# Optimization experiments

Hardware: AMD Instinct MI355X
Metric: run time of the kernel (lower is better)

## Reference

```python
import jax, jax.numpy as jnp
import numpy as np

K_FACTOR = 8
TOP_N = 4
NUM_LAYER = 2


def setup_inputs() -> dict:
    key = jax.random.key(0)
    ks = jax.random.split(key, 5)
    num_ent, num_rel, n_edges = 50000, 500, 500000
    emb_dim = 128
    emb_s = emb_dim // K_FACTOR  # 16
    ent_embeddings = jax.random.normal(ks[0], (num_ent, emb_dim), jnp.float32)
    rel_embeddings = jax.random.normal(ks[1], (num_rel, TOP_N * emb_s), jnp.float32)
    rel_att = jax.random.normal(ks[2], (num_rel, K_FACTOR), jnp.float32)
    edge_index = jax.random.randint(ks[3], (2, n_edges), 0, num_ent)
    edge_type = jax.random.randint(ks[4], (n_edges,), 0, num_rel)
    return dict(ent_embeddings=ent_embeddings, rel_embeddings=rel_embeddings,
                rel_att=rel_att, edge_index=edge_index, edge_type=edge_type,
                num_ent=num_ent, num_rel=num_rel)


def _segment_mean(src, idx, n):
    s = jax.ops.segment_sum(src, idx, num_segments=n)
    c = jax.ops.segment_sum(jnp.ones((src.shape[0],), src.dtype), idx, num_segments=n)
    return jnp.where(c[:, None] > 0, s / jnp.maximum(c, 1.0)[:, None], 0.0)


def _conv(x, r, r_att, ei, et, num_ent, num_rel):
    emb_dim = x.shape[1]
    s = emb_dim // K_FACTOR
    # add self-loop edges with relation id num_rel (zero embedding / zero att)
    loop = jnp.arange(num_ent, dtype=ei.dtype)
    ei = jnp.concatenate([ei, jnp.stack([loop, loop])], axis=1)
    et = jnp.concatenate([et, jnp.full((num_ent,), num_rel, et.dtype)])
    r_pad = jnp.concatenate([r, jnp.zeros((1, r.shape[1]), r.dtype)], axis=0)
    ra_pad = jnp.concatenate([r_att, jnp.zeros((1, K_FACTOR), r_att.dtype)], axis=0)

    neigh_t = x[ei[1]]          # (E, D)
    neigh_h = x[ei[0]]          # (E, D)
    neigh_r = r_pad[et]         # (E, top_n*s)
    att = jax.nn.softmax(ra_pad[et], axis=1)      # (E, k)
    order = jnp.argsort(-att, axis=-1)             # descending sort indices
    top, rem = order[:, :TOP_N], order[:, TOP_N:]

    E = neigh_h.shape[0]
    tf = neigh_t.reshape(E, K_FACTOR, s)
    hf = neigh_h.reshape(E, K_FACTOR, s)
    t_top = jnp.take_along_axis(tf, top[:, :, None], axis=1)  # (E, top_n, s)
    h_top = jnp.take_along_axis(hf, top[:, :, None], axis=1)
    h_rem = jnp.take_along_axis(hf, rem[:, :, None], axis=1)

    tmp = (h_top.reshape(E, -1) + neigh_r).reshape(E, TOP_N, s)
    rows = jnp.arange(E)[:, None]
    # the fresh random ent_embed in the original is fully overwritten by the
    # two scatters (top + remaining cover all k_factor slots) -> deterministic
    ent = (jnp.zeros((E, K_FACTOR, s), x.dtype)
           .at[rows, top].set(tmp)
           .at[rows, rem].set(h_rem))

    ent_embed = _segment_mean(ent.reshape(E, emb_dim), ei[1], num_ent)
    rel_embed = _segment_mean(t_top.reshape(E, -1) - h_top.reshape(E, -1), et, num_rel + 1)
    return jax.nn.relu(ent_embed), rel_embed[:-1], r_att


def reference(ent_embeddings, rel_embeddings, rel_att, edge_index, edge_type, num_ent, num_rel):
    x, r = ent_embeddings, rel_embeddings
    for _ in range(NUM_LAYER):
        # faithful to MAE.forward: the ORIGINAL rel_att is passed to every layer
        x, r, _ = _conv(x, r, rel_att, edge_index, edge_type, num_ent, num_rel)
    return (x, r)
```

## Files before the change

kernel.cpp:

```cpp
#include <hip/hip_runtime.h>

#define KF 8
#define TN 4
#define SDIM 16
#define EMB 128
#define NS 8
#define NB 128
#define NT 512
#define NRMAX 512
#define SCE 1024

typedef unsigned int u32;

__device__ __forceinline__ u32 pack2bf(float a, float b) {
    u32 ua = __float_as_uint(a), ub = __float_as_uint(b);
    ua = (ua + 0x7FFFu + ((ua >> 16) & 1u)) >> 16;
    ub = (ub + 0x7FFFu + ((ub >> 16) & 1u)) >> 16;
    return ua | (ub << 16);
}
__device__ __forceinline__ float lo16(u32 w) { return __uint_as_float(w << 16); }
__device__ __forceinline__ float hi16(u32 w) { return __uint_as_float(w & 0xFFFF0000u); }

__global__ __launch_bounds__(256) void k_init(int* __restrict__ deg, int num_ent,
                                              int* __restrict__ rcnt, int num_rel,
                                              float* __restrict__ rsumA, float* __restrict__ rsumB,
                                              int nrsum) {
    int i = blockIdx.x * 256 + threadIdx.x;
    if (i < num_ent) deg[i] = 0;
    if (i < num_rel) rcnt[i] = 0;
    if (i < nrsum) { rsumA[i] = 0.f; rsumB[i] = 0.f; }
}

__global__ __launch_bounds__(256) void k_hist(const int* __restrict__ tails, const int* __restrict__ types,
                                              int nE, int num_rel,
                                              int* __restrict__ deg, int* __restrict__ rcnt) {
    __shared__ int hist[NRMAX];
    for (int q = threadIdx.x; q < num_rel; q += 256) hist[q] = 0;
    __syncthreads();
    for (int i = blockIdx.x * 256 + threadIdx.x; i < nE; i += gridDim.x * 256) {
        atomicAdd(&deg[tails[i]], 1);
        atomicAdd(&hist[types[i]], 1);
    }
    __syncthreads();
    for (int q = threadIdx.x; q < num_rel; q += 256) {
        int h = hist[q];
        if (h) atomicAdd(&rcnt[q], h);
    }
}

__device__ void scan_small(const int* __restrict__ in, int* __restrict__ out, int* __restrict__ out2, int n) {
    __shared__ int warp_sums[16];
    int carry = 0;
    int lane = threadIdx.x & 63, wid = threadIdx.x >> 6;
    int nw = blockDim.x >> 6;
    for (int base = 0; base < n; base += blockDim.x) {
        int i = base + (int)threadIdx.x;
        int v = (i < n) ? in[i] : 0;
        int sv = v;
        for (int o = 1; o < 64; o <<= 1) { int t = __shfl_up(sv, o, 64); if (lane >= o) sv += t; }
        if (lane == 63) warp_sums[wid] = sv;
        __syncthreads();
        if (wid == 0 && lane < nw) {
            int ws = warp_sums[lane];
            for (int o = 1; o < 16; o <<= 1) { int t = __shfl_up(ws, o, 64); if (lane >= o) ws += t; }
            warp_sums[lane] = ws;
        }
        __syncthreads();
        int wofs = (wid > 0) ? warp_sums[wid - 1] : 0;
        int total = warp_sums[nw - 1];
        if (i < n) {
            int e = carry + wofs + sv - v;
            out[i] = e;
            if (out2) out2[i] = e;
        }
        carry += total;
        __syncthreads();
    }
    if (threadIdx.x == 0) out[n] = carry;
}

__global__ void k_scan_pair(const int* __restrict__ bsum, int* __restrict__ bofs, int nblk,
                            const int* __restrict__ rcnt, int* __restrict__ rel_off,
                            int* __restrict__ rel_cur, int num_rel) {
    if (blockIdx.x == 0) scan_small(bsum, bofs, nullptr, nblk);
    else                 scan_small(rcnt, rel_off, rel_cur, num_rel);
}

__global__ __launch_bounds__(256) void k_scan1(const int* __restrict__ in, int* __restrict__ out,
                                               int* __restrict__ bsum, int n) {
    __shared__ int warp_sums[4];
    int blk = blockIdx.x;
    int i0 = blk * SCE + (int)threadIdx.x * 4;
    int v[4];
#pragma unroll
    for (int j = 0; j < 4; ++j) { int i = i0 + j; v[j] = (i < n) ? in[i] : 0; }
    int tsum = v[0] + v[1] + v[2] + v[3];
    int lane = threadIdx.x & 63, wid = threadIdx.x >> 6;
    int sv = tsum;
    for (int o = 1; o < 64; o <<= 1) { int t = __shfl_up(sv, o, 64); if (lane >= o) sv += t; }
    if (lane == 63) warp_sums[wid] = sv;
    __syncthreads();
    if (threadIdx.x == 0) {
        int s = 0;
        for (int w = 0; w < 4; ++w) { int t = warp_sums[w]; warp_sums[w] = s; s += t; }
        bsum[blk] = s;
    }
    __syncthreads();
    int run = warp_sums[wid] + sv - tsum;
#pragma unroll
    for (int j = 0; j < 4; ++j) { int i = i0 + j; if (i < n) out[i] = run; run += v[j]; }
}

__global__ __launch_bounds__(256) void k_scan2(int* __restrict__ out, int* __restrict__ out2,
                                               const int* __restrict__ bofs, int n, int nblk) {
    int blk = blockIdx.x;
    int add = bofs[blk];
    int i0 = blk * SCE + (int)threadIdx.x * 4;
#pragma unroll
    for (int j = 0; j < 4; ++j) {
        int i = i0 + j;
        if (i < n) { int val = out[i] + add; out[i] = val; out2[i] = val; }
    }
    if (blk == 0 && threadIdx.x == 0) out[n] = bofs[nblk];
}

__global__ __launch_bounds__(256) void k_scatter_fused(
        const int* __restrict__ heads, const int* __restrict__ tails, const int* __restrict__ types,
        int nE, int num_ent, int num_rel,
        int* __restrict__ tail_cur, u32* __restrict__ tail_edges,
        int* __restrict__ rel_cur, u32* __restrict__ rel_edges,
        const float4* __restrict__ x4, u32* __restrict__ xh, int n4,
        const float* __restrict__ rel_att, const float* __restrict__ r0,
        int* __restrict__ posmap, int* __restrict__ topmap, u32* __restrict__ pr0,
        int nc, int np) {
    int bid = blockIdx.x;
    if (bid < NT) {
        int xcd = bid & 7;
        int w = bid >> 3;
        int nw = NT >> 3;
        int per = (num_ent + 7) >> 3;
        int lo = xcd * per, hi = min(lo + per, num_ent);
        for (int i = w * 256 + (int)threadIdx.x; i < nE; i += nw * 256) {
            int t = tails[i];
            if (t >= lo && t < hi) {
                int p = atomicAdd(&tail_cur[t], 1);
                tail_edges[p] = (u32)heads[i] | ((u32)types[i] << 16);
            }
        }
    } else if (bid < NT + NB) {
        __shared__ int hist[NRMAX];
        __shared__ int base[NRMAX];
        int bi = bid - NT;
        int c = (bi & 7) * (NB >> 3) + (bi >> 3);
        int chunk = (nE + NB - 1) / NB;
        int beg = c * chunk, end = min(beg + chunk, nE);
        for (int q = threadIdx.x; q < num_rel; q += 256) hist[q] = 0;
        __syncthreads();
        for (int i = beg + (int)threadIdx.x; i < end; i += 256) atomicAdd(&hist[types[i]], 1);
        __syncthreads();
        for (int q = threadIdx.x; q < num_rel; q += 256) {
            int h = hist[q];
            base[q] = h > 0 ? atomicAdd(&rel_cur[q], h) : 0;
            hist[q] = 0;
        }
        __syncthreads();
        for (int i = beg + (int)threadIdx.x; i < end; i += 256) {
            int q = types[i];
            int rank = atomicAdd(&hist[q], 1);
            rel_edges[base[q] + rank] = (u32)tails[i] | ((u32)heads[i] << 16);
        }
    } else if (bid < NT + NB + nc) {
        int i = (bid - NT - NB) * 256 + (int)threadIdx.x;
        if (i < n4) {
            float4 v = x4[i];
            ((uint2*)xh)[i] = make_uint2(pack2bf(v.x, v.y), pack2bf(v.z, v.w));
        }
    } else {
        int q = (bid - NT - NB - nc) * 4 + ((int)threadIdx.x >> 6);
        if (q >= num_rel) return;
        int i = threadIdx.x & 63;
        float v[KF]; int idx[KF];
        for (int k = 0; k < KF; ++k) { v[k] = rel_att[q * KF + k]; idx[k] = k; }
        for (int a = 1; a < KF; ++a) {
            float va = v[a]; int ia = idx[a]; int j = a - 1;
            while (j >= 0 && v[j] < va) { v[j + 1] = v[j]; idx[j + 1] = idx[j]; --j; }
            v[j + 1] = va; idx[j + 1] = ia;
        }
        int pos[KF];
        for (int k = 0; k < KF; ++k) pos[k] = -1;
        for (int j = 0; j < TN; ++j) pos[idx[j]] = j;
        if (i < KF) posmap[q * KF + i] = pos[i];
        if (i < TN) topmap[q * TN + i] = idx[i];
        int k = i >> 3;
        int p = pos[k];
        u32 w = 0;
        if (p >= 0) {
            float a = r0[q * 64 + p * SDIM + ((2 * i) & 15)];
            float b = r0[q * 64 + p * SDIM + ((2 * i + 1) & 15)];
            w = pack2bf(a, b);
        }
        pr0[q * 64 + i] = w;
    }
}

__global__ __launch_bounds__(256) void k_rel_pass(const u32* __restrict__ xh,
                                                  const int* __restrict__ rel_off,
                                                  const u32* __restrict__ rel_edges,
                                                  const int* __restrict__ topmap,
                                                  float* __restrict__ rsum_top) {
    int bid = blockIdx.x;
    int q = bid >> 3, s = bid & 7;
    int lane = threadIdx.x & 63;
    int qw = lane >> 4, c = lane & 15;
    int wid = threadIdx.x >> 6;
    int k = topmap[q * TN + (c >> 2)];
    int woff = k * 8 + (c & 3) * 2;
    int beg = rel_off[q], end = rel_off[q + 1];
    float acc[4] = {0.f, 0.f, 0.f, 0.f};
    for (int e = beg + s * 16 + wid * 4 + qw; e < end; e += 128) {
        u32 ew = rel_edges[e];
        int t = (int)(ew & 0xFFFFu);
        int h = (int)(ew >> 16);
        uint2 ta = *(const uint2*)(xh + ((size_t)t << 6) + woff);
        uint2 hb = *(const uint2*)(xh + ((size_t)h << 6) + woff);
        acc[0] += lo16(ta.x) - lo16(hb.x);
        acc[1] += hi16(ta.x) - hi16(hb.x);
        acc[2] += lo16(ta.y) - lo16(hb.y);
        acc[3] += hi16(ta.y) - hi16(hb.y);
    }
#pragma unroll
    for (int d = 0; d < 4; ++d) {
        acc[d] += __shfl_xor(acc[d], 16, 64);
        acc[d] += __shfl_xor(acc[d], 32, 64);
    }
    __shared__ float prt[4][64];
    if (qw == 0) {
#pragma unroll
        for (int d = 0; d < 4; ++d) prt[wid][c * 4 + d] = acc[d];
    }
    __syncthreads();
    int tid = threadIdx.x;
    if (tid < 64) {
        float v = prt[0][tid] + prt[1][tid] + prt[2][tid] + prt[3][tid];
        atomicAdd(&rsum_top[(size_t)q * 64 + tid], v);
    }
}

template <bool OUT_BF16>
__global__ __launch_bounds__(256) void k_ent_pass(const u32* __restrict__ xh, const u32* __restrict__ prh,
                                                  const int* __restrict__ tail_off,
                                                  const u32* __restrict__ tail_edges,
                                                  u32* __restrict__ xout_h, float4* __restrict__ xout_f,
                                                  int num_ent) {
    int wid = threadIdx.x >> 6;
    int t = blockIdx.x * 4 + wid;
    if (t >= num_ent) return;
    int lane = threadIdx.x & 63;
    int qw = lane >> 4, c = lane & 15;
    int beg = tail_off[t], end = tail_off[t + 1];
    int deg = end - beg;
    float acc[8] = {0.f, 0.f, 0.f, 0.f, 0.f, 0.f, 0.f, 0.f};
    for (int b2 = 0; b2 < deg; b2 += 64) {
        int m = min(64, deg - b2);
        u32 ew = (lane < m) ? tail_edges[beg + b2 + lane] : 0u;
        for (int j = 0; j < m; j += 4) {
            int idx = j + qw;
            u32 w = __shfl(ew, idx, 64);
            uint4 xr = make_uint4(0, 0, 0, 0), pr = make_uint4(0, 0, 0, 0);
            if (idx < m) {
                int h = (int)(w & 0xFFFFu);
                int q = (int)(w >> 16);
                xr = *(const uint4*)(xh + ((size_t)h << 6) + (c << 2));
                pr = *(const uint4*)(prh + ((size_t)q << 6) + (c << 2));
            }
            acc[0] += lo16(xr.x) + lo16(pr.x);
            acc[1] += hi16(xr.x) + hi16(pr.x);
            acc[2] += lo16(xr.y) + lo16(pr.y);
            acc[3] += hi16(xr.y) + hi16(pr.y);
            acc[4] += lo16(xr.z) + lo16(pr.z);
            acc[5] += hi16(xr.z) + hi16(pr.z);
            acc[6] += lo16(xr.w) + lo16(pr.w);
            acc[7] += hi16(xr.w) + hi16(pr.w);
        }
    }
#pragma unroll
    for (int d = 0; d < 8; ++d) {
        acc[d] += __shfl_xor(acc[d], 16, 64);
        acc[d] += __shfl_xor(acc[d], 32, 64);
    }
    if (qw == 0) {
        uint4 sw = *(const uint4*)(xh + ((size_t)t << 6) + (c << 2));
        float s[8] = { lo16(sw.x), hi16(sw.x), lo16(sw.y), hi16(sw.y),
                       lo16(sw.z), hi16(sw.z), lo16(sw.w), hi16(sw.w) };
        float inv = 1.f / (float)(deg + 1);
        float o[8];
#pragma unroll
        for (int d = 0; d < 8; ++d) {
            float v = (acc[d] + s[d]) * inv;
            o[d] = v > 0.f ? v : 0.f;
        }
        if (OUT_BF16) {
            uint4 ow = make_uint4(pack2bf(o[0], o[1]), pack2bf(o[2], o[3]),
                                  pack2bf(o[4], o[5]), pack2bf(o[6], o[7]));
            *(uint4*)(xout_h + ((size_t)t << 6) + (c << 2)) = ow;
        } else {
            xout_f[((size_t)t << 5) + (c << 1)]     = make_float4(o[0], o[1], o[2], o[3]);
            xout_f[((size_t)t << 5) + (c << 1) + 1] = make_float4(o[4], o[5], o[6], o[7]);
        }
    }
}

__global__ __launch_bounds__(64) void k_relfin_pr(const float* __restrict__ rsum_top,
                                                  const int* __restrict__ rel_off,
                                                  const int* __restrict__ posmap,
                                                  u32* __restrict__ prh, int num_rel) {
    int q = blockIdx.x;
    if (q >= num_rel) return;
    int i = threadIdx.x;
    int k = i >> 3;
    int pos = posmap[q * KF + k];
    int cnt = rel_off[q + 1] - rel_off[q];
    u32 w = 0;
    if (pos >= 0 && cnt > 0) {
        float inv = 1.f / (float)cnt;
        int d0 = (2 * i) & 15;
        float a = rsum_top[(size_t)q * 64 + pos * SDIM + d0] * inv;
        float b = rsum_top[(size_t)q * 64 + pos * SDIM + d0 + 1] * inv;
        w = pack2bf(a, b);
    }
    prh[q * 64 + i] = w;
}

__global__ __launch_bounds__(64) void k_relfin(const float* __restrict__ rsum_top,
                                               const int* __restrict__ rel_off,
                                               float* __restrict__ rout) {
    int q = blockIdx.x;
    int t = threadIdx.x;
    int cnt = rel_off[q + 1] - rel_off[q];
    rout[q * 64 + t] = cnt > 0 ? rsum_top[(size_t)q * 64 + t] / (float)cnt : 0.f;
}

extern "C" void kernel_launch(void* const* d_in, const int* in_sizes, int n_in,
                              void* d_out, int out_size, void* d_ws, size_t ws_size,
                              hipStream_t stream) {
    const float* x0 = (const float*)d_in[0];
    const float* r0 = (const float*)d_in[1];
    const float* rel_att = (const float*)d_in[2];
    const int* edge_index = (const int*)d_in[3];
    const int* edge_type = (const int*)d_in[4];

    const int num_ent = in_sizes[0] / EMB;
    const int num_rel = in_sizes[2] / KF;
    const int nE = in_sizes[4];

    const int* heads = edge_index;
    const int* tails = edge_index + nE;

    const int nblk = (num_ent + SCE - 1) / SCE;
    const int n4 = num_ent * 32;
    const int nc = (n4 + 255) / 256;
    const int np = (num_rel + 3) / 4;

    char* base = (char*)d_ws;
    size_t off = 0;
    auto carve = [&](size_t bytes) { char* p = base + off; off = (off + bytes + 255) & ~(size_t)255; return p; };
    int* deg        = (int*)carve((size_t)num_ent * 4);
    int* tail_off   = (int*)carve((size_t)(num_ent + 1) * 4);
    int* tail_cur   = (int*)carve((size_t)num_ent * 4);
    u32* tail_edges = (u32*)carve((size_t)nE * 4);
    int* rcnt       = (int*)carve((size_t)num_rel * 4);
    int* rel_off    = (int*)carve((size_t)(num_rel + 1) * 4);
    int* rel_cur    = (int*)carve((size_t)num_rel * 4);
    u32* rel_edges  = (u32*)carve((size_t)nE * 4);
    int* posmap     = (int*)carve((size_t)num_rel * KF * 4);
    int* topmap     = (int*)carve((size_t)num_rel * TN * 4);
    int* bsum       = (int*)carve((size_t)nblk * 4);
    int* bofs       = (int*)carve((size_t)(nblk + 1) * 4);
    u32* x0h        = (u32*)carve((size_t)num_ent * EMB * 2);
    u32* x1h        = (u32*)carve((size_t)num_ent * EMB * 2);
    u32* pr0        = (u32*)carve((size_t)num_rel * 64 * 4);
    u32* pr1        = (u32*)carve((size_t)num_rel * 64 * 4);
    float* rsumA    = (float*)carve((size_t)num_rel * 64 * 4);
    float* rsumB    = (float*)carve((size_t)num_rel * 64 * 4);
    (void)ws_size;

    float* x_out = (float*)d_out;
    float* r_out = (float*)d_out + (size_t)num_ent * EMB;

    int initmax = num_ent > num_rel * 64 ? num_ent : num_rel * 64;
    k_init<<<(initmax + 255) / 256, 256, 0, stream>>>(deg, num_ent, rcnt, num_rel,
                                                      rsumA, rsumB, num_rel * 64);
    k_hist<<<256, 256, 0, stream>>>(tails, edge_type, nE, num_rel, deg, rcnt);
    k_scan1<<<nblk, 256, 0, stream>>>(deg, tail_off, bsum, num_ent);
    k_scan_pair<<<2, 1024, 0, stream>>>(bsum, bofs, nblk, rcnt, rel_off, rel_cur, num_rel);
    k_scan2<<<nblk, 256, 0, stream>>>(tail_off, tail_cur, bofs, num_ent, nblk);
    k_scatter_fused<<<NT + NB + nc + np, 256, 0, stream>>>(
        heads, tails, edge_type, nE, num_ent, num_rel,
        tail_cur, tail_edges, rel_cur, rel_edges,
        (const float4*)x0, x0h, n4, rel_att, r0, posmap, topmap, pr0, nc, np);

    int egrid = (num_ent + 3) / 4;

    k_rel_pass<<<num_rel * NS, 256, 0, stream>>>(x0h, rel_off, rel_edges, topmap, rsumA);
    k_ent_pass<true><<<egrid, 256, 0, stream>>>(x0h, pr0, tail_off, tail_edges, x1h, nullptr, num_ent);
    k_relfin_pr<<<num_rel, 64, 0, stream>>>(rsumA, rel_off, posmap, pr1, num_rel);

    k_rel_pass<<<num_rel * NS, 256, 0, stream>>>(x1h, rel_off, rel_edges, topmap, rsumB);
    k_ent_pass<false><<<egrid, 256, 0, stream>>>(x1h, pr1, tail_off, tail_edges, nullptr, (float4*)x_out, num_ent);
    k_relfin<<<num_rel, 64, 0, stream>>>(rsumB, rel_off, r_out);
}
```

Measured before the change: 195.7 us.

## Fuse three-pass scan into decoupled-lookback scan and fold relation finalize into ent pass

Replaces the scan1/scan_pair/scan2 sequence with a single kernel that publishes per-block sums with flags and has each block spin on its predecessors, with one extra block doing the relation-count scan. The relation finalize kernels (relfin_pr, relfin) are folded into the tail of the entity-pass grids as extra blocks. This removes four kernel launches and their inter-kernel gaps. The spin-wait scan relies on earlier blocks being scheduled, and each block serially reads all prior block sums.

```diff
diff --git a/kernel.cpp b/kernel.cpp
--- a/kernel.cpp
+++ b/kernel.cpp
@@ -24,11 +24,12 @@
 __global__ __launch_bounds__(256) void k_init(int* __restrict__ deg, int num_ent,
                                               int* __restrict__ rcnt, int num_rel,
                                               float* __restrict__ rsumA, float* __restrict__ rsumB,
-                                              int nrsum) {
+                                              int nrsum, int* __restrict__ flags, int nblk) {
     int i = blockIdx.x * 256 + threadIdx.x;
     if (i < num_ent) deg[i] = 0;
     if (i < num_rel) rcnt[i] = 0;
     if (i < nrsum) { rsumA[i] = 0.f; rsumB[i] = 0.f; }
+    if (i < nblk) flags[i] = 0;
 }
 
 __global__ __launch_bounds__(256) void k_hist(const int* __restrict__ tails, const int* __restrict__ types,
@@ -79,49 +80,54 @@
     if (threadIdx.x == 0) out[n] = carry;
 }
 
-__global__ void k_scan_pair(const int* __restrict__ bsum, int* __restrict__ bofs, int nblk,
-                            const int* __restrict__ rcnt, int* __restrict__ rel_off,
-                            int* __restrict__ rel_cur, int num_rel) {
-    if (blockIdx.x == 0) scan_small(bsum, bofs, nullptr, nblk);
-    else                 scan_small(rcnt, rel_off, rel_cur, num_rel);
-}
-
-__global__ __launch_bounds__(256) void k_scan1(const int* __restrict__ in, int* __restrict__ out,
-                                               int* __restrict__ bsum, int n) {
-    __shared__ int warp_sums[4];
-    int blk = blockIdx.x;
-    int i0 = blk * SCE + (int)threadIdx.x * 4;
+__global__ __launch_bounds__(256) void k_scan_fused(const int* __restrict__ deg,
+                                                    int* __restrict__ tail_off, int* __restrict__ tail_cur,
+                                                    int n, int nblk,
+                                                    int* __restrict__ vals, int* __restrict__ flags,
+                                                    const int* __restrict__ rcnt, int* __restrict__ rel_off,
+                                                    int* __restrict__ rel_cur, int num_rel) {
+    int b = blockIdx.x;
+    if (b == nblk) { scan_small(rcnt, rel_off, rel_cur, num_rel); return; }
+    __shared__ int wsum[4];
+    __shared__ int pw[4];
+    __shared__ int sprefix;
+    int tid = threadIdx.x;
+    int lane = tid & 63, wid = tid >> 6;
+    int i0 = b * SCE + tid * 4;
     int v[4];
 #pragma unroll
-    for (int j = 0; j < 4; ++j) { int i = i0 + j; v[j] = (i < n) ? in[i] : 0; }
+    for (int j = 0; j < 4; ++j) { int i = i0 + j; v[j] = (i < n) ? deg[i] : 0; }
     int tsum = v[0] + v[1] + v[2] + v[3];
-    int lane = threadIdx.x & 63, wid = threadIdx.x >> 6;
     int sv = tsum;
     for (int o = 1; o < 64; o <<= 1) { int t = __shfl_up(sv, o, 64); if (lane >= o) sv += t; }
-    if (lane == 63) warp_sums[wid] = sv;
-    __syncthreads();
-    if (threadIdx.x == 0) {
+    if (lane == 63) wsum[wid] = sv;
+    __syncthreads();
+    if (tid == 0) {
         int s = 0;
-        for (int w = 0; w < 4; ++w) { int t = warp_sums[w]; warp_sums[w] = s; s += t; }
-        bsum[blk] = s;
-    }
-    __syncthreads();
-    int run = warp_sums[wid] + sv - tsum;
-#pragma unroll
-    for (int j = 0; j < 4; ++j) { int i = i0 + j; if (i < n) out[i] = run; run += v[j]; }
-}
-
-__global__ __launch_bounds__(256) void k_scan2(int* __restrict__ out, int* __restrict__ out2,
-                                               const int* __restrict__ bofs, int n, int nblk) {
-    int blk = blockIdx.x;
-    int add = bofs[blk];
-    int i0 = blk * SCE + (int)threadIdx.x * 4;
+        for (int w = 0; w < 4; ++w) { int t = wsum[w]; wsum[w] = s; s += t; }
+        vals[b] = s;
+        __threadfence();
+        atomicExch(&flags[b], 1);
+    }
+    __syncthreads();
+    int p = 0;
+    for (int i = tid; i < b; i += 256) {
+        while (atomicAdd(&flags[i], 0) == 0) {}
+        p += atomicAdd(&vals[i], 0);
+    }
+    for (int o = 1; o < 64; o <<= 1) p += __shfl_xor(p, o, 64);
+    if (lane == 0) pw[wid] = p;
+    __syncthreads();
+    if (tid == 0) sprefix = pw[0] + pw[1] + pw[2] + pw[3];
+    __syncthreads();
+    int run = sprefix + wsum[wid] + (sv - tsum);
 #pragma unroll
     for (int j = 0; j < 4; ++j) {
         int i = i0 + j;
-        if (i < n) { int val = out[i] + add; out[i] = val; out2[i] = val; }
-    }
-    if (blk == 0 && threadIdx.x == 0) out[n] = bofs[nblk];
+        if (i < n) { tail_off[i] = run; tail_cur[i] = run; }
+        run += v[j];
+    }
+    if (b == nblk - 1 && tid == 0) tail_off[n] = sprefix + vals[b];
 }
 
 __global__ __launch_bounds__(256) void k_scatter_fused(
@@ -251,9 +257,42 @@
                                                   const int* __restrict__ tail_off,
                                                   const u32* __restrict__ tail_edges,
                                                   u32* __restrict__ xout_h, float4* __restrict__ xout_f,
-                                                  int num_ent) {
+                                                  int num_ent, int egrid,
+                                                  const float* __restrict__ rsum_top,
+                                                  const int* __restrict__ rel_off,
+                                                  const int* __restrict__ posmap,
+                                                  u32* __restrict__ pr_out, float* __restrict__ rout,
+                                                  int num_rel) {
+    int bid = blockIdx.x;
+    if (bid >= egrid) {
+        if (OUT_BF16) {
+            int q = (bid - egrid) * 4 + ((int)threadIdx.x >> 6);
+            if (q >= num_rel) return;
+            int i = threadIdx.x & 63;
+            int k = i >> 3;
+            int pos = posmap[q * KF + k];
+            int cnt = rel_off[q + 1] - rel_off[q];
+            u32 w = 0;
+            if (pos >= 0 && cnt > 0) {
+                float inv = 1.f / (float)cnt;
+                int d0 = (2 * i) & 15;
+                float a = rsum_top[(size_t)q * 64 + pos * SDIM + d0] * inv;
+                float b = rsum_top[(size_t)q * 64 + pos * SDIM + d0 + 1] * inv;
+                w = pack2bf(a, b);
+            }
+            pr_out[q * 64 + i] = w;
+        } else {
+            int idx = (bid - egrid) * 256 + (int)threadIdx.x;
+            if (idx < num_rel * 64) {
+                int q = idx >> 6;
+                int cnt = rel_off[q + 1] - rel_off[q];
+                rout[idx] = cnt > 0 ? rsum_top[idx] / (float)cnt : 0.f;
+            }
+        }
+        return;
+    }
     int wid = threadIdx.x >> 6;
-    int t = blockIdx.x * 4 + wid;
+    int t = bid * 4 + wid;
     if (t >= num_ent) return;
     int lane = threadIdx.x & 63;
     int qw = lane >> 4, c = lane & 15;
@@ -310,36 +349,6 @@
     }
 }
 
-__global__ __launch_bounds__(64) void k_relfin_pr(const float* __restrict__ rsum_top,
-                                                  const int* __restrict__ rel_off,
-                                                  const int* __restrict__ posmap,
-                                                  u32* __restrict__ prh, int num_rel) {
-    int q = blockIdx.x;
-    if (q >= num_rel) return;
-    int i = threadIdx.x;
-    int k = i >> 3;
-    int pos = posmap[q * KF + k];
-    int cnt = rel_off[q + 1] - rel_off[q];
-    u32 w = 0;
-    if (pos >= 0 && cnt > 0) {
-        float inv = 1.f / (float)cnt;
-        int d0 = (2 * i) & 15;
-        float a = rsum_top[(size_t)q * 64 + pos * SDIM + d0] * inv;
-        float b = rsum_top[(size_t)q * 64 + pos * SDIM + d0 + 1] * inv;
-        w = pack2bf(a, b);
-    }
-    prh[q * 64 + i] = w;
-}
-
-__global__ __launch_bounds__(64) void k_relfin(const float* __restrict__ rsum_top,
-                                               const int* __restrict__ rel_off,
-                                               float* __restrict__ rout) {
-    int q = blockIdx.x;
-    int t = threadIdx.x;
-    int cnt = rel_off[q + 1] - rel_off[q];
-    rout[q * 64 + t] = cnt > 0 ? rsum_top[(size_t)q * 64 + t] / (float)cnt : 0.f;
-}
-
 extern "C" void kernel_launch(void* const* d_in, const int* in_sizes, int n_in,
                               void* d_out, int out_size, void* d_ws, size_t ws_size,
                               hipStream_t stream) {
@@ -374,8 +383,8 @@
     u32* rel_edges  = (u32*)carve((size_t)nE * 4);
     int* posmap     = (int*)carve((size_t)num_rel * KF * 4);
     int* topmap     = (int*)carve((size_t)num_rel * TN * 4);
-    int* bsum       = (int*)carve((size_t)nblk * 4);
-    int* bofs       = (int*)carve((size_t)(nblk + 1) * 4);
+    int* svals      = (int*)carve((size_t)nblk * 4);
+    int* sflags     = (int*)carve((size_t)nblk * 4);
     u32* x0h        = (u32*)carve((size_t)num_ent * EMB * 2);
     u32* x1h        = (u32*)carve((size_t)num_ent * EMB * 2);
     u32* pr0        = (u32*)carve((size_t)num_rel * 64 * 4);
@@ -389,23 +398,25 @@
 
     int initmax = num_ent > num_rel * 64 ? num_ent : num_rel * 64;
     k_init<<<(initmax + 255) / 256, 256, 0, stream>>>(deg, num_ent, rcnt, num_rel,
-                                                      rsumA, rsumB, num_rel * 64);
+                                                      rsumA, rsumB, num_rel * 64, sflags, nblk);
     k_hist<<<256, 256, 0, stream>>>(tails, edge_type, nE, num_rel, deg, rcnt);
-    k_scan1<<<nblk, 256, 0, stream>>>(deg, tail_off, bsum, num_ent);
-    k_scan_pair<<<2, 1024, 0, stream>>>(bsum, bofs, nblk, rcnt, rel_off, rel_cur, num_rel);
-    k_scan2<<<nblk, 256, 0, stream>>>(tail_off, tail_cur, bofs, num_ent, nblk);
+    k_scan_fused<<<nblk + 1, 256, 0, stream>>>(deg, tail_off, tail_cur, num_ent, nblk,
+                                               svals, sflags, rcnt, rel_off, rel_cur, num_rel);
     k_scatter_fused<<<NT + NB + nc + np, 256, 0, stream>>>(
         heads, tails, edge_type, nE, num_ent, num_rel,
         tail_cur, tail_edges, rel_cur, rel_edges,
         (const float4*)x0, x0h, n4, rel_att, r0, posmap, topmap, pr0, nc, np);
 
     int egrid = (num_ent + 3) / 4;
+    int nfin1 = (num_rel + 3) / 4;
+    int nfin2 = (num_rel * 64 + 255) / 256;
 
     k_rel_pass<<<num_rel * NS, 256, 0, stream>>>(x0h, rel_off, rel_edges, topmap, rsumA);
-    k_ent_pass<true><<<egrid, 256, 0, stream>>>(x0h, pr0, tail_off, tail_edges, x1h, nullptr, num_ent);
-    k_relfin_pr<<<num_rel, 64, 0, stream>>>(rsumA, rel_off, posmap, pr1, num_rel);
-
+    k_ent_pass<true><<<egrid + nfin1, 256, 0, stream>>>(x0h, pr0, tail_off, tail_edges,
+                                                        x1h, nullptr, num_ent, egrid,
+                                                        rsumA, rel_off, posmap, pr1, nullptr, num_rel);
     k_rel_pass<<<num_rel * NS, 256, 0, stream>>>(x1h, rel_off, rel_edges, topmap, rsumB);
-    k_ent_pass<false><<<egrid, 256, 0, stream>>>(x1h, pr1, tail_off, tail_edges, nullptr, (float4*)x_out, num_ent);
-    k_relfin<<<num_rel, 64, 0, stream>>>(rsumB, rel_off, r_out);
-}
+    k_ent_pass<false><<<egrid + nfin2, 256, 0, stream>>>(x1h, pr1, tail_off, tail_edges,
+                                                         nullptr, (float4*)x_out, num_ent, egrid,
+                                                         rsumB, rel_off, nullptr, nullptr, r_out, num_rel);
+}
```

Result: faster. 189.7 us (-3.0%).
